# Performance work log

Measured on AMD Instinct MI355X. Metric: run time of the kernel, lower is better.

The kernel has to match this reference:

```python
import jax, jax.numpy as jnp
import numpy as np

ANCHORS = np.array([[10.0, 13.0], [16.0, 30.0], [33.0, 23.0]], dtype=np.float32)
IMG_DIM = 608
NUM_CLASS = 80


def setup_inputs() -> dict:
    key = jax.random.key(0)
    nB, nA, nH, nW = 32, 3, 76, 76
    attrib = 5 + NUM_CLASS  # 85
    x = jax.random.normal(key, (nB, nA * attrib, nH, nW), dtype=jnp.float32)
    return {"x": x}


def reference(x):
    nB, C, nH, nW = x.shape
    nA = ANCHORS.shape[0]
    attrib = 5 + NUM_CLASS
    stride = IMG_DIM / nH  # 8.0
    anchors = jnp.asarray(ANCHORS) / stride  # [nA, 2] in grid units

    # [nB, nA, nH, nW, attrib]
    preds = x.reshape(nB, nA, attrib, nH, nW).transpose(0, 1, 3, 4, 2)

    # mesh grid of cell offsets: mesh_x varies along W, mesh_y along H
    mesh_x = jnp.arange(nW, dtype=x.dtype)[None, :]   # [1, nW]
    mesh_y = jnp.arange(nH, dtype=x.dtype)[:, None]   # [nH, 1]

    xy = jax.nn.sigmoid(preds[..., 0:2])
    bx = xy[..., 0] + mesh_x                            # broadcast over [nB,nA,nH,nW]
    by = xy[..., 1] + mesh_y
    wh = jnp.exp(preds[..., 2:4]) * anchors[None, :, None, None, :]

    conf = jax.nn.sigmoid(preds[..., 4:5])
    cls = jax.nn.sigmoid(preds[..., 5:])

    boxes = jnp.stack([bx, by], axis=-1)
    boxes = jnp.concatenate([boxes, wh], axis=-1) * stride  # [nB,nA,nH,nW,4]

    out = jnp.concatenate([boxes, conf, cls], axis=-1)      # [nB,nA,nH,nW,attrib]
    # permute(0,2,3,1,4) then flatten -> [nB, nH*nW*nA, attrib]
    out = out.transpose(0, 2, 3, 1, 4).reshape(nB, nA * nH * nW, attrib)
    return out
```

## Files before the change

### kernel.cpp

```cpp
#include <hip/hip_runtime.h>


typedef float f4 __attribute__((ext_vector_type(4)));

constexpr int NB = 32;
constexpr int NH = 76;
constexpr int NW = 76;
constexpr int C = 255;
constexpr int ROW_F4 = NW / 4;
constexpr int BLK_F4 = C * ROW_F4;
constexpr int TILES = NB * NH;
constexpr int NTH = 1024;
constexpr int KMAX = 5;
constexpr int GRID = 256;
constexpr float STRIDE = 8.0f;

__device__ __forceinline__ float sigmoidf_(float v) {
    return 1.0f / (1.0f + __expf(-v));
}

__global__ __launch_bounds__(NTH) void yolo_kernel(const f4* __restrict__ x4,
                                                   f4* __restrict__ out4) {
    __shared__ f4 buf[2][BLK_F4];

    const int tid = threadIdx.x;

    int offk[KMAX];
    int basek[KMAX];
    int modek[KMAX];
    float scalek[KMAX];
    float w0k[KMAX];
    bool act[KMAX];

#pragma unroll
    for (int k = 0; k < KMAX; ++k) {
        const int i = tid + k * NTH;
        act[k] = (i < BLK_F4);
        const int ii = act[k] ? i : 0;
        const int row = ii / ROW_F4;
        const int c = ii - row * ROW_F4;
        offk[k] = row * (NH * ROW_F4) + c;
        basek[k] = 4 * c * C + row;
        const int a = (row >= 170) ? 2 : ((row >= 85) ? 1 : 0);
        const int attr = row - 85 * a;
        int mode = 0;
        float sc = 0.0f;
        if (attr == 0) mode = 1;
        else if (attr == 1) mode = 2;
        else if (attr == 2) { mode = 3; sc = (a == 0) ? 10.f : ((a == 1) ? 16.f : 33.f); }
        else if (attr == 3) { mode = 3; sc = (a == 0) ? 13.f : ((a == 1) ? 30.f : 23.f); }
        modek[k] = mode;
        scalek[k] = sc;
        w0k[k] = (float)(4 * c);
    }

    f4 stage[KMAX];

    auto load_tile = [&](int t) {
        const int b = t / NH;
        const int h = t - b * NH;
        const size_t inb = (size_t)b * (C * NH * ROW_F4) + (size_t)h * ROW_F4;
#pragma unroll
        for (int k = 0; k < KMAX; ++k)
            if (act[k]) stage[k] = x4[inb + offk[k]];
    };

    auto transform_store = [&](int t, int nxt) {
        const float hf = (float)(t % NH);
        float* __restrict__ tb = (float*)buf[nxt];
#pragma unroll
        for (int k = 0; k < KMAX; ++k) {
            if (!act[k]) continue;
            const f4 v = stage[k];
            f4 r;
            if (modek[k] == 3) {
                r.x = __expf(v.x) * scalek[k];
                r.y = __expf(v.y) * scalek[k];
                r.z = __expf(v.z) * scalek[k];
                r.w = __expf(v.w) * scalek[k];
            } else {
                r.x = sigmoidf_(v.x);
                r.y = sigmoidf_(v.y);
                r.z = sigmoidf_(v.z);
                r.w = sigmoidf_(v.w);
                if (modek[k] == 1) {
                    r.x = (r.x + w0k[k]) * STRIDE;
                    r.y = (r.y + w0k[k] + 1.0f) * STRIDE;
                    r.z = (r.z + w0k[k] + 2.0f) * STRIDE;
                    r.w = (r.w + w0k[k] + 3.0f) * STRIDE;
                } else if (modek[k] == 2) {
                    r.x = (r.x + hf) * STRIDE;
                    r.y = (r.y + hf) * STRIDE;
                    r.z = (r.z + hf) * STRIDE;
                    r.w = (r.w + hf) * STRIDE;
                }
            }
            const int base = basek[k];
            tb[base]         = r.x;
            tb[base + C]     = r.y;
            tb[base + 2 * C] = r.z;
            tb[base + 3 * C] = r.w;
        }
    };

    int t = blockIdx.x;
    load_tile(t);
    transform_store(t, 0);
    __syncthreads();
    int cur = 0;

    while (true) {
        const int tn = t + GRID;
        const bool have_next = (tn < TILES);

        if (have_next) load_tile(tn);

        const size_t ob = (size_t)t * BLK_F4;
#pragma unroll
        for (int k = 0; k < KMAX; ++k) {
            const int i = tid + k * NTH;
            if (i < BLK_F4)
                __builtin_nontemporal_store(buf[cur][i], &out4[ob + i]);
        }

        if (!have_next) break;
        transform_store(tn, cur ^ 1);
        __syncthreads();
        cur ^= 1;
        t = tn;
    }
}

extern "C" void kernel_launch(void* const* d_in, const int* in_sizes, int n_in,
                              void* d_out, int out_size, void* d_ws, size_t ws_size,
                              hipStream_t stream) {
    const f4* x4 = (const f4*)d_in[0];
    f4* out4 = (f4*)d_out;
    yolo_kernel<<<GRID, NTH, 0, stream>>>(x4, out4);
}
```

Baseline: 73.29 us.

## Single-buffer LDS, double grid, and map tiles per XCD for locality

Replaces the double-buffered shared tile with a single buffer. This halves LDS use so two 1024-thread blocks can reside per CU, and the grid is doubled to 512 blocks. Tiles are assigned in contiguous ranges per XCD (blockIdx & 7) to improve L2 locality, with a load-transform-sync-write schedule that prefetches the next tile into registers before the store phase. The trade-off is an extra barrier per tile and less intra-block overlap between LDS writes and global stores.

```diff
diff --git a/kernel.cpp b/kernel.cpp
--- a/kernel.cpp
+++ b/kernel.cpp
@@ -12,31 +12,32 @@
 constexpr int TILES = NB * NH;
 constexpr int NTH = 1024;
 constexpr int KMAX = 5;
-constexpr int GRID = 256;
+constexpr int TAIL = BLK_F4 - 4 * NTH;
+constexpr int GRID = 512;
+constexpr int NXCD = 8;
+constexpr int PER_XCD = TILES / NXCD;
+constexpr int BLKS_PER_XCD = GRID / NXCD;
 constexpr float STRIDE = 8.0f;
 
 __device__ __forceinline__ float sigmoidf_(float v) {
     return 1.0f / (1.0f + __expf(-v));
 }
 
-__global__ __launch_bounds__(NTH) void yolo_kernel(const f4* __restrict__ x4,
-                                                   f4* __restrict__ out4) {
-    __shared__ f4 buf[2][BLK_F4];
+__global__ __launch_bounds__(NTH, 8) void yolo_kernel(const f4* __restrict__ x4,
+                                                      f4* __restrict__ out4) {
+    __shared__ f4 buf[BLK_F4];
 
     const int tid = threadIdx.x;
 
     int offk[KMAX];
     int basek[KMAX];
     int modek[KMAX];
-    float scalek[KMAX];
-    float w0k[KMAX];
-    bool act[KMAX];
+    float auxk[KMAX];
 
 #pragma unroll
     for (int k = 0; k < KMAX; ++k) {
         const int i = tid + k * NTH;
-        act[k] = (i < BLK_F4);
-        const int ii = act[k] ? i : 0;
+        const int ii = (k < 4 || tid < TAIL) ? i : 0;
         const int row = ii / ROW_F4;
         const int c = ii - row * ROW_F4;
         offk[k] = row * (NH * ROW_F4) + c;
@@ -44,50 +45,58 @@
         const int a = (row >= 170) ? 2 : ((row >= 85) ? 1 : 0);
         const int attr = row - 85 * a;
         int mode = 0;
-        float sc = 0.0f;
+        float aux = (float)(4 * c);
         if (attr == 0) mode = 1;
         else if (attr == 1) mode = 2;
-        else if (attr == 2) { mode = 3; sc = (a == 0) ? 10.f : ((a == 1) ? 16.f : 33.f); }
-        else if (attr == 3) { mode = 3; sc = (a == 0) ? 13.f : ((a == 1) ? 30.f : 23.f); }
+        else if (attr == 2) { mode = 3; aux = (a == 0) ? 10.f : ((a == 1) ? 16.f : 33.f); }
+        else if (attr == 3) { mode = 3; aux = (a == 0) ? 13.f : ((a == 1) ? 30.f : 23.f); }
         modek[k] = mode;
-        scalek[k] = sc;
-        w0k[k] = (float)(4 * c);
+        auxk[k] = aux;
     }
+
+    const int x = blockIdx.x & (NXCD - 1);
+    const int j = blockIdx.x >> 3;
+    const int base_t = x * PER_XCD;
+    const int ntile = 4 + (j < (PER_XCD - 4 * BLKS_PER_XCD) ? 1 : 0);
 
     f4 stage[KMAX];
 
-    auto load_tile = [&](int t) {
+    auto issue = [&](int t) {
         const int b = t / NH;
         const int h = t - b * NH;
         const size_t inb = (size_t)b * (C * NH * ROW_F4) + (size_t)h * ROW_F4;
 #pragma unroll
         for (int k = 0; k < KMAX; ++k)
-            if (act[k]) stage[k] = x4[inb + offk[k]];
+            if (k < 4 || tid < TAIL) stage[k] = x4[inb + offk[k]];
     };
 
-    auto transform_store = [&](int t, int nxt) {
+    int t = base_t + j;
+    issue(t);
+    int idx = 0;
+    float* __restrict__ tb = (float*)buf;
+
+    while (true) {
         const float hf = (float)(t % NH);
-        float* __restrict__ tb = (float*)buf[nxt];
 #pragma unroll
         for (int k = 0; k < KMAX; ++k) {
-            if (!act[k]) continue;
+            if (!(k < 4 || tid < TAIL)) continue;
             const f4 v = stage[k];
             f4 r;
             if (modek[k] == 3) {
-                r.x = __expf(v.x) * scalek[k];
-                r.y = __expf(v.y) * scalek[k];
-                r.z = __expf(v.z) * scalek[k];
-                r.w = __expf(v.w) * scalek[k];
+                r.x = __expf(v.x) * auxk[k];
+                r.y = __expf(v.y) * auxk[k];
+                r.z = __expf(v.z) * auxk[k];
+                r.w = __expf(v.w) * auxk[k];
             } else {
                 r.x = sigmoidf_(v.x);
                 r.y = sigmoidf_(v.y);
                 r.z = sigmoidf_(v.z);
                 r.w = sigmoidf_(v.w);
                 if (modek[k] == 1) {
-                    r.x = (r.x + w0k[k]) * STRIDE;
-                    r.y = (r.y + w0k[k] + 1.0f) * STRIDE;
-                    r.z = (r.z + w0k[k] + 2.0f) * STRIDE;
-                    r.w = (r.w + w0k[k] + 3.0f) * STRIDE;
+                    r.x = (r.x + auxk[k]) * STRIDE;
+                    r.y = (r.y + auxk[k] + 1.0f) * STRIDE;
+                    r.z = (r.z + auxk[k] + 2.0f) * STRIDE;
+                    r.w = (r.w + auxk[k] + 3.0f) * STRIDE;
                 } else if (modek[k] == 2) {
                     r.x = (r.x + hf) * STRIDE;
                     r.y = (r.y + hf) * STRIDE;
@@ -95,39 +104,40 @@
                     r.w = (r.w + hf) * STRIDE;
                 }
             }
+            stage[k] = r;
+        }
+
+        if (idx > 0) __syncthreads();
+
+#pragma unroll
+        for (int k = 0; k < KMAX; ++k) {
+            if (!(k < 4 || tid < TAIL)) continue;
+            const f4 r = stage[k];
             const int base = basek[k];
             tb[base]         = r.x;
             tb[base + C]     = r.y;
             tb[base + 2 * C] = r.z;
             tb[base + 3 * C] = r.w;
         }
-    };
-
-    int t = blockIdx.x;
-    load_tile(t);
-    transform_store(t, 0);
-    __syncthreads();
-    int cur = 0;
-
-    while (true) {
-        const int tn = t + GRID;
-        const bool have_next = (tn < TILES);
-
-        if (have_next) load_tile(tn);
 
         const size_t ob = (size_t)t * BLK_F4;
+        ++idx;
+        const bool more = (idx < ntile);
+        if (more) {
+            t = base_t + idx * BLKS_PER_XCD + j;
+            issue(t);
+        }
+
+        __syncthreads();
+
 #pragma unroll
         for (int k = 0; k < KMAX; ++k) {
             const int i = tid + k * NTH;
-            if (i < BLK_F4)
-                __builtin_nontemporal_store(buf[cur][i], &out4[ob + i]);
+            if (k < 4 || tid < TAIL)
+                __builtin_nontemporal_store(buf[i], &out4[ob + i]);
         }
 
-        if (!have_next) break;
-        transform_store(tn, cur ^ 1);
-        __syncthreads();
-        cur ^= 1;
-        t = tn;
+        if (!more) break;
     }
 }
 
```

After: 70.61 us. 3.7% less time.
